# Performance work log

Measured on AMD Instinct MI355X. Metric: run time of the kernel, lower is better.

The kernel has to match this reference:

```python
import jax, jax.numpy as jnp
import numpy as np
from math import sqrt

KEY_DIM = 128
VALUE_DIM = 128
SUMMARY_DIM = 128
QUESTION_NUM = 10000
CONCEPT_NUM = 64
B = 128
S = 128


def setup_inputs() -> dict:
    key = jax.random.key(0)
    ks = jax.random.split(key, 24)
    stdev = 1.0 / sqrt(CONCEPT_NUM + KEY_DIM)

    def lin_w(k, out_f, in_f):
        bound = 1.0 / sqrt(in_f)
        return jax.random.uniform(k, (out_f, in_f), jnp.float32, -bound, bound)

    def lin_b(k, out_f, in_f):
        bound = 1.0 / sqrt(in_f)
        return jax.random.uniform(k, (out_f,), jnp.float32, -bound, bound)

    q_emb = jax.random.normal(ks[0], (QUESTION_NUM + 1, KEY_DIM), jnp.float32)
    q_emb = q_emb.at[0].set(0.0)  # padding_idx = 0
    i_emb = jax.random.normal(ks[1], (2 * QUESTION_NUM + 1, VALUE_DIM), jnp.float32)
    i_emb = i_emb.at[0].set(0.0)

    inp = {
        "right_input": jax.random.randint(ks[2], (B, S), 0, 2 * QUESTION_NUM + 1),
        "wrong_input": jax.random.randint(ks[3], (B, S), 0, 2 * QUESTION_NUM + 1),
        "target_id": jax.random.randint(ks[4], (B,), 0, QUESTION_NUM + 1),
        "q_emb": q_emb,
        "i_emb": i_emb,
        "key_W": lin_w(ks[5], CONCEPT_NUM, KEY_DIM),  # no bias
        "erase_W": lin_w(ks[6], VALUE_DIM, VALUE_DIM),
        "erase_b": lin_b(ks[7], VALUE_DIM, VALUE_DIM),
        "add_W": lin_w(ks[8], VALUE_DIM, VALUE_DIM),
        "add_b": lin_b(ks[9], VALUE_DIM, VALUE_DIM),
        "rsum_W": lin_w(ks[10], SUMMARY_DIM, VALUE_DIM + KEY_DIM),
        "rsum_b": lin_b(ks[11], SUMMARY_DIM, VALUE_DIM + KEY_DIM),
        "wsum_W": lin_w(ks[12], SUMMARY_DIM, VALUE_DIM + KEY_DIM),
        "wsum_b": lin_b(ks[13], SUMMARY_DIM, VALUE_DIM + KEY_DIM),
        "succ_W": lin_w(ks[14], 1, SUMMARY_DIM),
        "succ_b": lin_b(ks[15], 1, SUMMARY_DIM),
        "fail_W": lin_w(ks[16], 1, SUMMARY_DIM),
        "fail_b": lin_b(ks[17], 1, SUMMARY_DIM),
        "diff_W": lin_w(ks[18], 1, KEY_DIM),
        "diff_b": lin_b(ks[19], 1, KEY_DIM),
        "right_mem_init": jax.random.uniform(ks[20], (VALUE_DIM, CONCEPT_NUM), jnp.float32, -stdev, stdev),
        "wrong_mem_init": jax.random.uniform(ks[21], (VALUE_DIM, CONCEPT_NUM), jnp.float32, -stdev, stdev),
    }
    return inp


def reference(right_input, wrong_input, target_id, q_emb, i_emb, key_W,
              erase_W, erase_b, add_W, add_b, rsum_W, rsum_b, wsum_W, wsum_b,
              succ_W, succ_b, fail_W, fail_b, diff_W, diff_b,
              right_mem_init, wrong_mem_init):
    Q = (i_emb.shape[0] - 1) // 2
    batch = right_input.shape[0]

    def corr(qid):  # (B,) -> (B, C) correlation weights
        return jax.nn.softmax(q_emb[qid] @ key_W.T, axis=-1)

    def update(mem, inter):
        # mem: (B, V, C); inter: (B,) interaction ids
        vec = i_emb[inter]                                  # (B, V)
        e = jax.nn.sigmoid(vec @ erase_W.T + erase_b)       # (B, V)
        a = jnp.tanh(vec @ add_W.T + add_b)                 # (B, V)
        qid = inter - Q * (inter > Q).astype(inter.dtype)
        w = corr(qid)                                       # (B, C)
        # erase/add are outer products w (x) e, w (x) a -> (B, V, C)
        return mem * (1.0 - e[:, :, None] * w[:, None, :]) + a[:, :, None] * w[:, None, :]

    def step(carry, xs):
        rm, wm = carry
        ri, wi = xs
        return (update(rm, ri), update(wm, wi)), None

    rm0 = jnp.broadcast_to(right_mem_init, (batch,) + right_mem_init.shape)
    wm0 = jnp.broadcast_to(wrong_mem_init, (batch,) + wrong_mem_init.shape)
    (rm, wm), _ = jax.lax.scan(step, (rm0, wm0), (right_input.T, wrong_input.T))

    qv = q_emb[target_id]                                   # (B, K)
    w_t = corr(target_id)                                   # (B, C)
    right_read = jnp.einsum('bvc,bc->bv', rm, w_t)          # (B, V)
    wrong_read = jnp.einsum('bvc,bc->bv', wm, w_t)

    r_sum = jnp.tanh(jnp.concatenate([right_read, qv], axis=-1) @ rsum_W.T + rsum_b)
    w_sum = jnp.tanh(jnp.concatenate([wrong_read, qv], axis=-1) @ wsum_W.T + wsum_b)

    success_level = jnp.tanh(r_sum @ succ_W.T + succ_b)     # (B, 1)
    failure_level = jnp.tanh(w_sum @ fail_W.T + fail_b)     # (B, 1)
    difficulty_level = jnp.tanh(qv @ diff_W.T + diff_b)     # (B, 1)

    success_count = jnp.sum(jnp.clip(right_input, 0, 1)).astype(jnp.float32)
    failure_count = jnp.sum(jnp.clip(wrong_input, 0, 1)).astype(jnp.float32)

    out = (success_level * jax.nn.sigmoid(success_count)
           + failure_level * jax.nn.sigmoid(failure_count)
           - difficulty_level * 2.0)
    return out
```

## Files before the change

kernel.cpp:

```cpp
#include <hip/hip_runtime.h>
#include <hip/hip_bf16.h>

#define BB 128
#define SS 128
#define VD 128
#define CN 64
#define KD 128
#define QN 10000

typedef __attribute__((ext_vector_type(8))) short bf16x8;
typedef __attribute__((ext_vector_type(4))) float f32x4;

__device__ __forceinline__ float bflo(unsigned int u) { return __uint_as_float(u << 16); }
__device__ __forceinline__ float bfhi(unsigned int u) { return __uint_as_float(u & 0xffff0000u); }
__device__ __forceinline__ unsigned short f2bf(float f) {
    unsigned int x = __float_as_uint(f);
    return (unsigned short)((x + 0x7fffu + ((x >> 16) & 1u)) >> 16);
}
__device__ __forceinline__ unsigned int pk2(float lo, float hi) {
    return (unsigned int)f2bf(lo) | ((unsigned int)f2bf(hi) << 16);
}
__device__ __forceinline__ float fast_tanh(float x) {
    float e = __expf(2.0f * x);
    return 1.0f - 2.0f / (e + 1.0f);
}
__device__ __forceinline__ float fast_sig(float x) {
    return 1.0f / (1.0f + __expf(-x));
}

__global__ __launch_bounds__(256) void k_wcnt(
    const float* __restrict__ erase_W, const float* __restrict__ add_W,
    const float* __restrict__ key_W, unsigned short* __restrict__ Bfrag,
    const int* __restrict__ ri, const int* __restrict__ wi, float* __restrict__ sig)
{
    if (blockIdx.x < 20) {
        const int bid = blockIdx.x * 4 + (threadIdx.x >> 6);
        const int l = threadIdx.x & 63;
        const int n = (bid >> 2) * 16 + (l & 15);
        const int k0 = (bid & 3) * 32 + (l >> 4) * 8;
        const float* src;
        if (n < 128)      src = erase_W + (size_t)n * KD + k0;
        else if (n < 256) src = add_W + (size_t)(n - 128) * KD + k0;
        else              src = key_W + (size_t)(n - 256) * KD + k0;
        float4 fa = ((const float4*)src)[0];
        float4 fb = ((const float4*)src)[1];
        uint4 o = make_uint4(pk2(fa.x, fa.y), pk2(fa.z, fa.w), pk2(fb.x, fb.y), pk2(fb.z, fb.w));
        *(uint4*)(Bfrag + ((size_t)bid * 64 + l) * 8) = o;
    } else {
        __shared__ int sr_s[4], sw_s[4];
        const int t = threadIdx.x;
        const int4* r4 = (const int4*)ri;
        const int4* w4 = (const int4*)wi;
        int sr = 0, sw = 0;
        #pragma unroll 4
        for (int p = 0; p < 16; ++p) {
            int4 a = r4[p * 256 + t];
            int4 b = w4[p * 256 + t];
            sr += (a.x >= 1) + (a.y >= 1) + (a.z >= 1) + (a.w >= 1);
            sw += (b.x >= 1) + (b.y >= 1) + (b.z >= 1) + (b.w >= 1);
        }
        for (int off = 1; off < 64; off <<= 1) { sr += __shfl_xor(sr, off); sw += __shfl_xor(sw, off); }
        int wid = t >> 6;
        if ((t & 63) == 0) { sr_s[wid] = sr; sw_s[wid] = sw; }
        __syncthreads();
        if (t == 0) {
            int SR = sr_s[0]+sr_s[1]+sr_s[2]+sr_s[3];
            int SW = sw_s[0]+sw_s[1]+sw_s[2]+sw_s[3];
            sig[0] = 1.0f / (1.0f + __expf(-(float)SR));
            sig[1] = 1.0f / (1.0f + __expf(-(float)SW));
        }
    }
}

__global__ __launch_bounds__(512, 2) void k_chain(
    const int* __restrict__ ri, const int* __restrict__ wi, const int* __restrict__ tgt,
    const float* __restrict__ q_emb, const float* __restrict__ i_emb,
    const float* __restrict__ key_W,
    const float* __restrict__ erase_b, const float* __restrict__ add_b,
    const unsigned short* __restrict__ Bfrag,
    const float* __restrict__ rmem0, const float* __restrict__ wmem0,
    float* __restrict__ readbuf)
{
    __shared__ __align__(16) unsigned int lds_ea[SS * VD];
    __shared__ __align__(16) char xab[32 * 1024];
    __shared__ __align__(16) float logits[SS * 68];
    __shared__ __align__(16) unsigned short lds_w[SS * CN];
    __shared__ float q_t[KD];
    __shared__ float logit_t[CN];
    __shared__ float wt_lds[CN];
    __shared__ int qid_s[SS], ir_s[SS];
    __shared__ float psum[8 * 64];

    const int t = threadIdx.x;
    const int lane = t & 63;
    const int w = t >> 6;
    const int chain = blockIdx.x;
    const int m = chain >> 7;
    const int b = chain & 127;

    if (t < SS) {
        int inter = (m == 0 ? ri : wi)[b * SS + t];
        ir_s[t] = inter;
        qid_s[t] = (inter > QN) ? inter - QN : inter;
        q_t[t] = q_emb[(size_t)tgt[b] * KD + t];
    }
    __syncthreads();

    {
        const int r0 = t >> 3, o = t & 7;
        #pragma unroll
        for (int h = 0; h < 2; ++h) {
            const int r = r0 + h * 64;
            const float* src = q_emb + (size_t)qid_s[r] * KD + o * 16;
            float4 f0 = ((const float4*)src)[0];
            float4 f1 = ((const float4*)src)[1];
            float4 f2 = ((const float4*)src)[2];
            float4 f3 = ((const float4*)src)[3];
            const int bb = r * 256 + o * 32;
            const int sw = (r & 7) << 4;
            *(uint4*)(xab + (bb ^ sw))        = make_uint4(pk2(f0.x,f0.y), pk2(f0.z,f0.w), pk2(f1.x,f1.y), pk2(f1.z,f1.w));
            *(uint4*)(xab + ((bb + 16) ^ sw)) = make_uint4(pk2(f2.x,f2.y), pk2(f2.z,f2.w), pk2(f3.x,f3.y), pk2(f3.z,f3.w));
        }
        const int c = t >> 3, oct = t & 7;
        const float* kw = key_W + (size_t)c * KD + oct * 16;
        float s = 0.f;
        #pragma unroll
        for (int i = 0; i < 16; ++i) s = fmaf(kw[i], q_t[oct * 16 + i], s);
        s += __shfl_xor(s, 1); s += __shfl_xor(s, 2); s += __shfl_xor(s, 4);
        if (oct == 0) logit_t[c] = s;
    }
    __syncthreads();

    const int rowl = lane & 15;
    const int kb16 = (lane >> 4) * 16;
    const int rb4 = (lane >> 4) * 4;

    {
        if (w == 0) {
            float x = logit_t[lane];
            float mx = x;
            #pragma unroll
            for (int off = 1; off < 64; off <<= 1) mx = fmaxf(mx, __shfl_xor(mx, off));
            float e = __expf(x - mx);
            float ssum = e;
            #pragma unroll
            for (int off = 1; off < 64; off <<= 1) ssum += __shfl_xor(ssum, off);
            wt_lds[lane] = e / ssum;
        }
        bf16x8 afQ[4];
        const int row = w * 16 + rowl;
        #pragma unroll
        for (int kt = 0; kt < 4; ++kt)
            afQ[kt] = *(const bf16x8*)(xab + ((row * 256 + kt * 64 + kb16) ^ ((row & 7) << 4)));
        #pragma unroll
        for (int nt = 0; nt < 4; ++nt) {
            f32x4 acc = {0.f,0.f,0.f,0.f};
            #pragma unroll
            for (int kt = 0; kt < 4; ++kt) {
                bf16x8 bf = *(const bf16x8*)(Bfrag + ((size_t)((16 + nt) * 4 + kt) * 64 + lane) * 8);
                acc = __builtin_amdgcn_mfma_f32_16x16x32_bf16(afQ[kt], bf, acc, 0, 0, 0);
            }
            #pragma unroll
            for (int rr = 0; rr < 4; ++rr)
                logits[(w * 16 + rb4 + rr) * 68 + nt * 16 + rowl] = acc[rr];
        }
    }
    __syncthreads();

    {
        const int r0 = t >> 3, o = t & 7;
        uint4 xi[2][2];
        #pragma unroll
        for (int h = 0; h < 2; ++h) {
            const int r = r0 + h * 64;
            const float* src = i_emb + (size_t)ir_s[r] * KD + o * 16;
            float4 f0 = ((const float4*)src)[0];
            float4 f1 = ((const float4*)src)[1];
            float4 f2 = ((const float4*)src)[2];
            float4 f3 = ((const float4*)src)[3];
            xi[h][0] = make_uint4(pk2(f0.x,f0.y), pk2(f0.z,f0.w), pk2(f1.x,f1.y), pk2(f1.z,f1.w));
            xi[h][1] = make_uint4(pk2(f2.x,f2.y), pk2(f2.z,f2.w), pk2(f3.x,f3.y), pk2(f3.z,f3.w));
        }

        const int rr = t >> 2, q4 = t & 3;
        const float* L = logits + rr * 68 + q4 * 16;
        float4 va = ((const float4*)L)[0];
        float4 vb = ((const float4*)L)[1];
        float4 vc = ((const float4*)L)[2];
        float4 vd = ((const float4*)L)[3];
        float mx = fmaxf(fmaxf(fmaxf(va.x, va.y), fmaxf(va.z, va.w)),
                         fmaxf(fmaxf(vb.x, vb.y), fmaxf(vb.z, vb.w)));
        mx = fmaxf(mx, fmaxf(fmaxf(fmaxf(vc.x, vc.y), fmaxf(vc.z, vc.w)),
                             fmaxf(fmaxf(vd.x, vd.y), fmaxf(vd.z, vd.w))));
        mx = fmaxf(mx, __shfl_xor(mx, 1));
        mx = fmaxf(mx, __shfl_xor(mx, 2));
        float ex[16];
        ex[0] = __expf(va.x - mx); ex[1] = __expf(va.y - mx); ex[2] = __expf(va.z - mx); ex[3] = __expf(va.w - mx);
        ex[4] = __expf(vb.x - mx); ex[5] = __expf(vb.y - mx); ex[6] = __expf(vb.z - mx); ex[7] = __expf(vb.w - mx);
        ex[8] = __expf(vc.x - mx); ex[9] = __expf(vc.y - mx); ex[10] = __expf(vc.z - mx); ex[11] = __expf(vc.w - mx);
        ex[12] = __expf(vd.x - mx); ex[13] = __expf(vd.y - mx); ex[14] = __expf(vd.z - mx); ex[15] = __expf(vd.w - mx);
        float s = 0.f;
        #pragma unroll
        for (int i = 0; i < 16; ++i) s += ex[i];
        s += __shfl_xor(s, 1);
        s += __shfl_xor(s, 2);
        float inv = 1.0f / s;
        uint4 o0 = make_uint4(pk2(ex[0]*inv, ex[1]*inv), pk2(ex[2]*inv, ex[3]*inv),
                              pk2(ex[4]*inv, ex[5]*inv), pk2(ex[6]*inv, ex[7]*inv));
        uint4 o1 = make_uint4(pk2(ex[8]*inv, ex[9]*inv), pk2(ex[10]*inv, ex[11]*inv),
                              pk2(ex[12]*inv, ex[13]*inv), pk2(ex[14]*inv, ex[15]*inv));
        *(uint4*)(lds_w + rr * CN + q4 * 16)     = o0;
        *(uint4*)(lds_w + rr * CN + q4 * 16 + 8) = o1;

        #pragma unroll
        for (int h = 0; h < 2; ++h) {
            const int r = r0 + h * 64;
            const int bb = r * 256 + o * 32;
            const int sw = (r & 7) << 4;
            *(uint4*)(xab + (bb ^ sw))        = xi[h][0];
            *(uint4*)(xab + ((bb + 16) ^ sw)) = xi[h][1];
        }
    }
    __syncthreads();

    {
        bf16x8 afI[4];
        const int row = w * 16 + rowl;
        #pragma unroll
        for (int kt = 0; kt < 4; ++kt)
            afI[kt] = *(const bf16x8*)(xab + ((row * 256 + kt * 64 + kb16) ^ ((row & 7) << 4)));
        #pragma unroll
        for (int ci = 0; ci < 8; ++ci) {
            f32x4 ae = {0.f,0.f,0.f,0.f}, aa = {0.f,0.f,0.f,0.f};
            #pragma unroll
            for (int kt = 0; kt < 4; ++kt) {
                bf16x8 be = *(const bf16x8*)(Bfrag + ((size_t)(ci * 4 + kt) * 64 + lane) * 8);
                bf16x8 ba = *(const bf16x8*)(Bfrag + ((size_t)((8 + ci) * 4 + kt) * 64 + lane) * 8);
                ae = __builtin_amdgcn_mfma_f32_16x16x32_bf16(afI[kt], be, ae, 0, 0, 0);
                aa = __builtin_amdgcn_mfma_f32_16x16x32_bf16(afI[kt], ba, aa, 0, 0, 0);
            }
            const int cc = ci * 16 + rowl;
            const float bvE = erase_b[cc];
            const float bvA = add_b[cc];
            #pragma unroll
            for (int rr = 0; rr < 4; ++rr) {
                float e = fast_sig(ae[rr] + bvE);
                float a = fast_tanh(aa[rr] + bvA);
                lds_ea[(w * 16 + rb4 + rr) * VD + cc] = pk2(e, a);
            }
        }
    }

    const int vhalf = w & 1;
    const int cq = w >> 1;
    const int vg = lane >> 2;
    const int cg = lane & 3;
    const int v0 = vhalf * 64 + vg * 4;
    const int c0 = cq * 16 + cg * 4;
    const float* minit = (m == 0) ? rmem0 : wmem0;
    float mm[4][4];
    #pragma unroll
    for (int j = 0; j < 4; ++j) {
        float4 mi = *(const float4*)(minit + (v0 + j) * CN + c0);
        mm[j][0] = mi.x; mm[j][1] = mi.y; mm[j][2] = mi.z; mm[j][3] = mi.w;
    }
    __syncthreads();

    for (int so = 0; so < 16; ++so) {
        #pragma unroll
        for (int kk = 0; kk < 8; ++kk) {
            const int s = so * 8 + kk;
            uint4 ea = *(const uint4*)(lds_ea + s * VD + v0);
            uint2 wu = *(const uint2*)(lds_w + s * CN + c0);
            float e[4] = { bflo(ea.x), bflo(ea.y), bflo(ea.z), bflo(ea.w) };
            float a[4] = { bfhi(ea.x), bfhi(ea.y), bfhi(ea.z), bfhi(ea.w) };
            float wv[4] = { bflo(wu.x), bfhi(wu.x), bflo(wu.y), bfhi(wu.y) };
            #pragma unroll
            for (int j = 0; j < 4; ++j) {
                #pragma unroll
                for (int k = 0; k < 4; ++k) {
                    float g = fmaf(-e[j], mm[j][k], a[j]);
                    mm[j][k] = fmaf(wv[k], g, mm[j][k]);
                }
            }
        }
    }

    float4 wt = *(const float4*)(wt_lds + c0);
    float p[4];
    #pragma unroll
    for (int j = 0; j < 4; ++j) {
        float x = mm[j][0] * wt.x;
        x = fmaf(mm[j][1], wt.y, x);
        x = fmaf(mm[j][2], wt.z, x);
        x = fmaf(mm[j][3], wt.w, x);
        p[j] = x;
    }
    #pragma unroll
    for (int j = 0; j < 4; ++j) {
        p[j] += __shfl_xor(p[j], 1);
        p[j] += __shfl_xor(p[j], 2);
    }
    if (cg == 0) {
        #pragma unroll
        for (int j = 0; j < 4; ++j) psum[w * 64 + vg * 4 + j] = p[j];
    }
    __syncthreads();
    if (t < 128) {
        const int vh = t >> 6, vl = t & 63;
        float s = psum[(0 * 2 + vh) * 64 + vl] + psum[(1 * 2 + vh) * 64 + vl]
                + psum[(2 * 2 + vh) * 64 + vl] + psum[(3 * 2 + vh) * 64 + vl];
        readbuf[(size_t)chain * VD + t] = s;
    }
}

__global__ __launch_bounds__(256) void k_head(
    const float* __restrict__ readbuf, const int* __restrict__ tgt,
    const float* __restrict__ q_emb,
    const float* __restrict__ rsum_W, const float* __restrict__ rsum_b,
    const float* __restrict__ wsum_W, const float* __restrict__ wsum_b,
    const float* __restrict__ succ_W, const float* __restrict__ succ_b,
    const float* __restrict__ fail_W, const float* __restrict__ fail_b,
    const float* __restrict__ diff_W, const float* __restrict__ diff_b,
    const float* __restrict__ sig, float* __restrict__ out)
{
    __shared__ float xr[256], xw[256];
    __shared__ float part[2][128];
    __shared__ float red_s[6];
    const int t = threadIdx.x;
    const int j = t & 127;
    const int h = t >> 7;
    const int b = blockIdx.x;
    if (h == 0) {
        int tid_ = tgt[b];
        float qv = q_emb[(size_t)tid_ * KD + j];
        xr[j]       = readbuf[(size_t)b * VD + j];
        xr[128 + j] = qv;
        xw[j]       = readbuf[(size_t)(BB + b) * VD + j];
        xw[128 + j] = qv;
    }
    __syncthreads();

    float rs = (h == 0) ? rsum_b[j] : 0.0f;
    float wv = (h == 0) ? wsum_b[j] : 0.0f;
    const float* rw = rsum_W + (size_t)j * 256 + h * 128;
    const float* ww = wsum_W + (size_t)j * 256 + h * 128;
    const float* xrp = xr + h * 128;
    const float* xwp = xw + h * 128;
    #pragma unroll 4
    for (int k = 0; k < 128; ++k) {
        rs = fmaf(rw[k], xrp[k], rs);
        wv = fmaf(ww[k], xwp[k], wv);
    }
    if (h == 1) { part[0][j] = rs; part[1][j] = wv; }
    __syncthreads();
    if (h == 0) {
        rs += part[0][j];
        wv += part[1][j];
        float r_sum = fast_tanh(rs), w_sum = fast_tanh(wv);
        float qv = xr[128 + j];
        float ps = r_sum * succ_W[j];
        float pf = w_sum * fail_W[j];
        float pd = qv    * diff_W[j];
        for (int off = 1; off < 64; off <<= 1) {
            ps += __shfl_xor(ps, off);
            pf += __shfl_xor(pf, off);
            pd += __shfl_xor(pd, off);
        }
        int wid = j >> 6;
        if ((j & 63) == 0) { red_s[wid*3+0] = ps; red_s[wid*3+1] = pf; red_s[wid*3+2] = pd; }
    }
    __syncthreads();
    if (t == 0) {
        float Ps = red_s[0] + red_s[3];
        float Pf = red_s[1] + red_s[4];
        float Pd = red_s[2] + red_s[5];
        float succ = fast_tanh(Ps + succ_b[0]);
        float fail = fast_tanh(Pf + fail_b[0]);
        float diff = fast_tanh(Pd + diff_b[0]);
        out[b] = succ * sig[0] + fail * sig[1] - 2.0f * diff;
    }
}

extern "C" void kernel_launch(void* const* d_in, const int* in_sizes, int n_in,
                              void* d_out, int out_size, void* d_ws, size_t ws_size,
                              hipStream_t stream) {
    const int*   ri      = (const int*)d_in[0];
    const int*   wi      = (const int*)d_in[1];
    const int*   tgt     = (const int*)d_in[2];
    const float* q_emb   = (const float*)d_in[3];
    const float* i_emb   = (const float*)d_in[4];
    const float* key_W   = (const float*)d_in[5];
    const float* erase_W = (const float*)d_in[6];
    const float* erase_b = (const float*)d_in[7];
    const float* add_W   = (const float*)d_in[8];
    const float* add_b   = (const float*)d_in[9];
    const float* rsum_W  = (const float*)d_in[10];
    const float* rsum_b  = (const float*)d_in[11];
    const float* wsum_W  = (const float*)d_in[12];
    const float* wsum_b  = (const float*)d_in[13];
    const float* succ_W  = (const float*)d_in[14];
    const float* succ_b  = (const float*)d_in[15];
    const float* fail_W  = (const float*)d_in[16];
    const float* fail_b  = (const float*)d_in[17];
    const float* diff_W  = (const float*)d_in[18];
    const float* diff_b  = (const float*)d_in[19];
    const float* rmem0   = (const float*)d_in[20];
    const float* wmem0   = (const float*)d_in[21];

    char* ws = (char*)d_ws;
    float*          readbuf = (float*)(ws + 0);
    unsigned short* Bfrag   = (unsigned short*)(ws + 131072);
    float*          sig     = (float*)(ws + 212992);
    float*          out     = (float*)d_out;

    hipLaunchKernelGGL(k_wcnt, dim3(21), dim3(256), 0, stream,
        erase_W, add_W, key_W, Bfrag, ri, wi, sig);
    hipLaunchKernelGGL(k_chain, dim3(256), dim3(512), 0, stream,
        ri, wi, tgt, q_emb, i_emb, key_W, erase_b, add_b, Bfrag,
        rmem0, wmem0, readbuf);
    hipLaunchKernelGGL(k_head, dim3(128), dim3(256), 0, stream,
        readbuf, tgt, q_emb, rsum_W, rsum_b, wsum_W, wsum_b,
        succ_W, succ_b, fail_W, fail_b, diff_W, diff_b, sig, out);
}
```

Measured before the change: 50.58 us.

## Double k_chain block to 1024 threads and alias LDS buffers

Raises the chain kernel's block from 512 to 1024 threads, so each thread in the serial memory-update loop holds 2x4 state elements instead of 4x4, halving the per-thread dependency chain. The MFMA stages are split so waves share row tiles but divide the column tiles, and the xab/logits/lds_ea buffers are overlaid in one shared region to fit the larger block. The psum reduction is replaced by a 16-lane shuffle reduction with direct global writes. Costs include an extra barrier, more register pressure under the tighter launch bound, and more LDS loads per useful FMA in the recurrence.

Result: slower. 52.14 us (+3.1%).

```diff
diff --git a/kernel.cpp b/kernel.cpp
--- a/kernel.cpp
+++ b/kernel.cpp
@@ -72,7 +72,7 @@
     }
 }
 
-__global__ __launch_bounds__(512, 2) void k_chain(
+__global__ __launch_bounds__(1024, 4) void k_chain(
     const int* __restrict__ ri, const int* __restrict__ wi, const int* __restrict__ tgt,
     const float* __restrict__ q_emb, const float* __restrict__ i_emb,
     const float* __restrict__ key_W,
@@ -81,15 +81,16 @@
     const float* __restrict__ rmem0, const float* __restrict__ wmem0,
     float* __restrict__ readbuf)
 {
-    __shared__ __align__(16) unsigned int lds_ea[SS * VD];
-    __shared__ __align__(16) char xab[32 * 1024];
-    __shared__ __align__(16) float logits[SS * 68];
+    __shared__ __align__(16) char U[32768 + 34816];
     __shared__ __align__(16) unsigned short lds_w[SS * CN];
     __shared__ float q_t[KD];
     __shared__ float logit_t[CN];
     __shared__ float wt_lds[CN];
     __shared__ int qid_s[SS], ir_s[SS];
-    __shared__ float psum[8 * 64];
+
+    char* xab = U;
+    float* logits = (float*)(U + 32768);
+    unsigned int* lds_ea = (unsigned int*)U;
 
     const int t = threadIdx.x;
     const int lane = t & 63;
@@ -107,33 +108,32 @@
     __syncthreads();
 
     {
-        const int r0 = t >> 3, o = t & 7;
-        #pragma unroll
-        for (int h = 0; h < 2; ++h) {
-            const int r = r0 + h * 64;
-            const float* src = q_emb + (size_t)qid_s[r] * KD + o * 16;
-            float4 f0 = ((const float4*)src)[0];
-            float4 f1 = ((const float4*)src)[1];
-            float4 f2 = ((const float4*)src)[2];
-            float4 f3 = ((const float4*)src)[3];
-            const int bb = r * 256 + o * 32;
-            const int sw = (r & 7) << 4;
-            *(uint4*)(xab + (bb ^ sw))        = make_uint4(pk2(f0.x,f0.y), pk2(f0.z,f0.w), pk2(f1.x,f1.y), pk2(f1.z,f1.w));
-            *(uint4*)(xab + ((bb + 16) ^ sw)) = make_uint4(pk2(f2.x,f2.y), pk2(f2.z,f2.w), pk2(f3.x,f3.y), pk2(f3.z,f3.w));
-        }
-        const int c = t >> 3, oct = t & 7;
-        const float* kw = key_W + (size_t)c * KD + oct * 16;
-        float s = 0.f;
-        #pragma unroll
-        for (int i = 0; i < 16; ++i) s = fmaf(kw[i], q_t[oct * 16 + i], s);
-        s += __shfl_xor(s, 1); s += __shfl_xor(s, 2); s += __shfl_xor(s, 4);
-        if (oct == 0) logit_t[c] = s;
+        const int r = t >> 3, o = t & 7;
+        const float* src = q_emb + (size_t)qid_s[r] * KD + o * 16;
+        float4 f0 = ((const float4*)src)[0];
+        float4 f1 = ((const float4*)src)[1];
+        float4 f2 = ((const float4*)src)[2];
+        float4 f3 = ((const float4*)src)[3];
+        const int bb = r * 256 + o * 32;
+        const int sw = (r & 7) << 4;
+        *(uint4*)(xab + (bb ^ sw))        = make_uint4(pk2(f0.x,f0.y), pk2(f0.z,f0.w), pk2(f1.x,f1.y), pk2(f1.z,f1.w));
+        *(uint4*)(xab + ((bb + 16) ^ sw)) = make_uint4(pk2(f2.x,f2.y), pk2(f2.z,f2.w), pk2(f3.x,f3.y), pk2(f3.z,f3.w));
+        if (t < 512) {
+            const int c = t >> 3, oct = t & 7;
+            const float* kw = key_W + (size_t)c * KD + oct * 16;
+            float s = 0.f;
+            #pragma unroll
+            for (int i = 0; i < 16; ++i) s = fmaf(kw[i], q_t[oct * 16 + i], s);
+            s += __shfl_xor(s, 1); s += __shfl_xor(s, 2); s += __shfl_xor(s, 4);
+            if (oct == 0) logit_t[c] = s;
+        }
     }
     __syncthreads();
 
     const int rowl = lane & 15;
     const int kb16 = (lane >> 4) * 16;
     const int rb4 = (lane >> 4) * 4;
+    const int rt = w & 7;
 
     {
         if (w == 0) {
@@ -148,12 +148,14 @@
             wt_lds[lane] = e / ssum;
         }
         bf16x8 afQ[4];
-        const int row = w * 16 + rowl;
+        const int row = rt * 16 + rowl;
         #pragma unroll
         for (int kt = 0; kt < 4; ++kt)
             afQ[kt] = *(const bf16x8*)(xab + ((row * 256 + kt * 64 + kb16) ^ ((row & 7) << 4)));
-        #pragma unroll
-        for (int nt = 0; nt < 4; ++nt) {
+        const int nt0 = (w >> 3) * 2;
+        #pragma unroll
+        for (int ni = 0; ni < 2; ++ni) {
+            const int nt = nt0 + ni;
             f32x4 acc = {0.f,0.f,0.f,0.f};
             #pragma unroll
             for (int kt = 0; kt < 4; ++kt) {
@@ -162,75 +164,56 @@
             }
             #pragma unroll
             for (int rr = 0; rr < 4; ++rr)
-                logits[(w * 16 + rb4 + rr) * 68 + nt * 16 + rowl] = acc[rr];
-        }
-    }
-    __syncthreads();
-
-    {
-        const int r0 = t >> 3, o = t & 7;
-        uint4 xi[2][2];
-        #pragma unroll
-        for (int h = 0; h < 2; ++h) {
-            const int r = r0 + h * 64;
-            const float* src = i_emb + (size_t)ir_s[r] * KD + o * 16;
-            float4 f0 = ((const float4*)src)[0];
-            float4 f1 = ((const float4*)src)[1];
-            float4 f2 = ((const float4*)src)[2];
-            float4 f3 = ((const float4*)src)[3];
-            xi[h][0] = make_uint4(pk2(f0.x,f0.y), pk2(f0.z,f0.w), pk2(f1.x,f1.y), pk2(f1.z,f1.w));
-            xi[h][1] = make_uint4(pk2(f2.x,f2.y), pk2(f2.z,f2.w), pk2(f3.x,f3.y), pk2(f3.z,f3.w));
-        }
-
-        const int rr = t >> 2, q4 = t & 3;
-        const float* L = logits + rr * 68 + q4 * 16;
+                logits[(rt * 16 + rb4 + rr) * 68 + nt * 16 + rowl] = acc[rr];
+        }
+    }
+    __syncthreads();
+
+    {
+        const int rr = t >> 3, q = t & 7;
+        const float* L = logits + rr * 68 + q * 8;
         float4 va = ((const float4*)L)[0];
         float4 vb = ((const float4*)L)[1];
-        float4 vc = ((const float4*)L)[2];
-        float4 vd = ((const float4*)L)[3];
         float mx = fmaxf(fmaxf(fmaxf(va.x, va.y), fmaxf(va.z, va.w)),
                          fmaxf(fmaxf(vb.x, vb.y), fmaxf(vb.z, vb.w)));
-        mx = fmaxf(mx, fmaxf(fmaxf(fmaxf(vc.x, vc.y), fmaxf(vc.z, vc.w)),
-                             fmaxf(fmaxf(vd.x, vd.y), fmaxf(vd.z, vd.w))));
         mx = fmaxf(mx, __shfl_xor(mx, 1));
         mx = fmaxf(mx, __shfl_xor(mx, 2));
-        float ex[16];
-        ex[0] = __expf(va.x - mx); ex[1] = __expf(va.y - mx); ex[2] = __expf(va.z - mx); ex[3] = __expf(va.w - mx);
-        ex[4] = __expf(vb.x - mx); ex[5] = __expf(vb.y - mx); ex[6] = __expf(vb.z - mx); ex[7] = __expf(vb.w - mx);
-        ex[8] = __expf(vc.x - mx); ex[9] = __expf(vc.y - mx); ex[10] = __expf(vc.z - mx); ex[11] = __expf(vc.w - mx);
-        ex[12] = __expf(vd.x - mx); ex[13] = __expf(vd.y - mx); ex[14] = __expf(vd.z - mx); ex[15] = __expf(vd.w - mx);
-        float s = 0.f;
-        #pragma unroll
-        for (int i = 0; i < 16; ++i) s += ex[i];
-        s += __shfl_xor(s, 1);
-        s += __shfl_xor(s, 2);
+        mx = fmaxf(mx, __shfl_xor(mx, 4));
+        float e0 = __expf(va.x - mx), e1 = __expf(va.y - mx), e2 = __expf(va.z - mx), e3 = __expf(va.w - mx);
+        float e4 = __expf(vb.x - mx), e5 = __expf(vb.y - mx), e6 = __expf(vb.z - mx), e7 = __expf(vb.w - mx);
+        float s = e0 + e1 + e2 + e3 + e4 + e5 + e6 + e7;
+        s += __shfl_xor(s, 1); s += __shfl_xor(s, 2); s += __shfl_xor(s, 4);
         float inv = 1.0f / s;
-        uint4 o0 = make_uint4(pk2(ex[0]*inv, ex[1]*inv), pk2(ex[2]*inv, ex[3]*inv),
-                              pk2(ex[4]*inv, ex[5]*inv), pk2(ex[6]*inv, ex[7]*inv));
-        uint4 o1 = make_uint4(pk2(ex[8]*inv, ex[9]*inv), pk2(ex[10]*inv, ex[11]*inv),
-                              pk2(ex[12]*inv, ex[13]*inv), pk2(ex[14]*inv, ex[15]*inv));
-        *(uint4*)(lds_w + rr * CN + q4 * 16)     = o0;
-        *(uint4*)(lds_w + rr * CN + q4 * 16 + 8) = o1;
-
-        #pragma unroll
-        for (int h = 0; h < 2; ++h) {
-            const int r = r0 + h * 64;
-            const int bb = r * 256 + o * 32;
-            const int sw = (r & 7) << 4;
-            *(uint4*)(xab + (bb ^ sw))        = xi[h][0];
-            *(uint4*)(xab + ((bb + 16) ^ sw)) = xi[h][1];
-        }
-    }
-    __syncthreads();
-
-    {
-        bf16x8 afI[4];
-        const int row = w * 16 + rowl;
+        uint4 o = make_uint4(pk2(e0*inv, e1*inv), pk2(e2*inv, e3*inv),
+                             pk2(e4*inv, e5*inv), pk2(e6*inv, e7*inv));
+        *(uint4*)(lds_w + rr * CN + q * 8) = o;
+
+        const float* src = i_emb + (size_t)ir_s[rr] * KD + q * 16;
+        float4 f0 = ((const float4*)src)[0];
+        float4 f1 = ((const float4*)src)[1];
+        float4 f2 = ((const float4*)src)[2];
+        float4 f3 = ((const float4*)src)[3];
+        const int bb = rr * 256 + q * 32;
+        const int sw = (rr & 7) << 4;
+        *(uint4*)(xab + (bb ^ sw))        = make_uint4(pk2(f0.x,f0.y), pk2(f0.z,f0.w), pk2(f1.x,f1.y), pk2(f1.z,f1.w));
+        *(uint4*)(xab + ((bb + 16) ^ sw)) = make_uint4(pk2(f2.x,f2.y), pk2(f2.z,f2.w), pk2(f3.x,f3.y), pk2(f3.z,f3.w));
+    }
+    __syncthreads();
+
+    bf16x8 afI[4];
+    {
+        const int row = rt * 16 + rowl;
         #pragma unroll
         for (int kt = 0; kt < 4; ++kt)
             afI[kt] = *(const bf16x8*)(xab + ((row * 256 + kt * 64 + kb16) ^ ((row & 7) << 4)));
-        #pragma unroll
-        for (int ci = 0; ci < 8; ++ci) {
+    }
+    __syncthreads();
+
+    {
+        const int ci0 = (w >> 3) * 4;
+        #pragma unroll
+        for (int ii = 0; ii < 4; ++ii) {
+            const int ci = ci0 + ii;
             f32x4 ae = {0.f,0.f,0.f,0.f}, aa = {0.f,0.f,0.f,0.f};
             #pragma unroll
             for (int kt = 0; kt < 4; ++kt) {
@@ -246,71 +229,61 @@
             for (int rr = 0; rr < 4; ++rr) {
                 float e = fast_sig(ae[rr] + bvE);
                 float a = fast_tanh(aa[rr] + bvA);
-                lds_ea[(w * 16 + rb4 + rr) * VD + cc] = pk2(e, a);
+                lds_ea[(rt * 16 + rb4 + rr) * VD + cc] = pk2(e, a);
             }
         }
     }
 
-    const int vhalf = w & 1;
-    const int cq = w >> 1;
-    const int vg = lane >> 2;
-    const int cg = lane & 3;
-    const int v0 = vhalf * 64 + vg * 4;
-    const int c0 = cq * 16 + cg * 4;
+    const int v0 = (t >> 4) * 2;
+    const int c0 = (t & 15) * 4;
     const float* minit = (m == 0) ? rmem0 : wmem0;
-    float mm[4][4];
-    #pragma unroll
-    for (int j = 0; j < 4; ++j) {
-        float4 mi = *(const float4*)(minit + (v0 + j) * CN + c0);
-        mm[j][0] = mi.x; mm[j][1] = mi.y; mm[j][2] = mi.z; mm[j][3] = mi.w;
-    }
-    __syncthreads();
-
+    float mm0[4], mm1[4];
+    {
+        float4 a0 = *(const float4*)(minit + (v0 + 0) * CN + c0);
+        float4 a1 = *(const float4*)(minit + (v0 + 1) * CN + c0);
+        mm0[0] = a0.x; mm0[1] = a0.y; mm0[2] = a0.z; mm0[3] = a0.w;
+        mm1[0] = a1.x; mm1[1] = a1.y; mm1[2] = a1.z; mm1[3] = a1.w;
+    }
+    __syncthreads();
+
+    const unsigned int* ea_base = lds_ea + v0;
+    const unsigned short* w_base = lds_w + c0;
     for (int so = 0; so < 16; ++so) {
         #pragma unroll
         for (int kk = 0; kk < 8; ++kk) {
             const int s = so * 8 + kk;
-            uint4 ea = *(const uint4*)(lds_ea + s * VD + v0);
-            uint2 wu = *(const uint2*)(lds_w + s * CN + c0);
-            float e[4] = { bflo(ea.x), bflo(ea.y), bflo(ea.z), bflo(ea.w) };
-            float a[4] = { bfhi(ea.x), bfhi(ea.y), bfhi(ea.z), bfhi(ea.w) };
-            float wv[4] = { bflo(wu.x), bfhi(wu.x), bflo(wu.y), bfhi(wu.y) };
-            #pragma unroll
-            for (int j = 0; j < 4; ++j) {
-                #pragma unroll
-                for (int k = 0; k < 4; ++k) {
-                    float g = fmaf(-e[j], mm[j][k], a[j]);
-                    mm[j][k] = fmaf(wv[k], g, mm[j][k]);
-                }
-            }
-        }
-    }
-
-    float4 wt = *(const float4*)(wt_lds + c0);
-    float p[4];
-    #pragma unroll
-    for (int j = 0; j < 4; ++j) {
-        float x = mm[j][0] * wt.x;
-        x = fmaf(mm[j][1], wt.y, x);
-        x = fmaf(mm[j][2], wt.z, x);
-        x = fmaf(mm[j][3], wt.w, x);
-        p[j] = x;
-    }
-    #pragma unroll
-    for (int j = 0; j < 4; ++j) {
-        p[j] += __shfl_xor(p[j], 1);
-        p[j] += __shfl_xor(p[j], 2);
-    }
-    if (cg == 0) {
-        #pragma unroll
-        for (int j = 0; j < 4; ++j) psum[w * 64 + vg * 4 + j] = p[j];
-    }
-    __syncthreads();
-    if (t < 128) {
-        const int vh = t >> 6, vl = t & 63;
-        float s = psum[(0 * 2 + vh) * 64 + vl] + psum[(1 * 2 + vh) * 64 + vl]
-                + psum[(2 * 2 + vh) * 64 + vl] + psum[(3 * 2 + vh) * 64 + vl];
-        readbuf[(size_t)chain * VD + t] = s;
+            uint2 ea = *(const uint2*)(ea_base + s * VD);
+            uint2 wu = *(const uint2*)(w_base + s * CN);
+            float e0 = bflo(ea.x), a0 = bfhi(ea.x);
+            float e1 = bflo(ea.y), a1 = bfhi(ea.y);
+            float w0 = bflo(wu.x), w1 = bfhi(wu.x), w2 = bflo(wu.y), w3 = bfhi(wu.y);
+            float g;
+            g = fmaf(-e0, mm0[0], a0); mm0[0] = fmaf(w0, g, mm0[0]);
+            g = fmaf(-e0, mm0[1], a0); mm0[1] = fmaf(w1, g, mm0[1]);
+            g = fmaf(-e0, mm0[2], a0); mm0[2] = fmaf(w2, g, mm0[2]);
+            g = fmaf(-e0, mm0[3], a0); mm0[3] = fmaf(w3, g, mm0[3]);
+            g = fmaf(-e1, mm1[0], a1); mm1[0] = fmaf(w0, g, mm1[0]);
+            g = fmaf(-e1, mm1[1], a1); mm1[1] = fmaf(w1, g, mm1[1]);
+            g = fmaf(-e1, mm1[2], a1); mm1[2] = fmaf(w2, g, mm1[2]);
+            g = fmaf(-e1, mm1[3], a1); mm1[3] = fmaf(w3, g, mm1[3]);
+        }
+    }
+
+    {
+        float4 wt = *(const float4*)(wt_lds + c0);
+        float p0 = mm0[0] * wt.x;
+        p0 = fmaf(mm0[1], wt.y, p0); p0 = fmaf(mm0[2], wt.z, p0); p0 = fmaf(mm0[3], wt.w, p0);
+        float p1 = mm1[0] * wt.x;
+        p1 = fmaf(mm1[1], wt.y, p1); p1 = fmaf(mm1[2], wt.z, p1); p1 = fmaf(mm1[3], wt.w, p1);
+        #pragma unroll
+        for (int off = 1; off < 16; off <<= 1) {
+            p0 += __shfl_xor(p0, off);
+            p1 += __shfl_xor(p1, off);
+        }
+        if ((t & 15) == 0) {
+            readbuf[(size_t)chain * VD + v0]     = p0;
+            readbuf[(size_t)chain * VD + v0 + 1] = p1;
+        }
     }
 }
 
@@ -416,7 +389,7 @@
 
     hipLaunchKernelGGL(k_wcnt, dim3(21), dim3(256), 0, stream,
         erase_W, add_W, key_W, Bfrag, ri, wi, sig);
-    hipLaunchKernelGGL(k_chain, dim3(256), dim3(512), 0, stream,
+    hipLaunchKernelGGL(k_chain, dim3(256), dim3(1024), 0, stream,
         ri, wi, tgt, q_emb, i_emb, key_W, erase_b, add_b, Bfrag,
         rmem0, wmem0, readbuf);
     hipLaunchKernelGGL(k_head, dim3(128), dim3(256), 0, stream,
```

## Double k_chain block to 1024 threads, splitting gather and MFMA phases

Applied to the files above, without the earlier changes.

Launches k_chain with 1024 threads instead of 512. The embedding gathers, softmax and MFMA projection phases are split across 16 waves, each doing half the previous per-thread work, while the serial memory recurrence still runs on the first 512 threads. The aim is to cut latency in the gather- and MFMA-bound prologue that runs before the recurrence. It also replaces the hand-written bf16 rounding with the library packed float2-to-bf16 conversion. Raising launch bounds to (1024,4) may tighten the register budget and cause spills in the recurrence, and half the threads sit idle during the main loop.

Result: no change. 50.16 us (median of 2 runs) (-0.8%).

```diff
diff --git a/kernel.cpp b/kernel.cpp
--- a/kernel.cpp
+++ b/kernel.cpp
@@ -13,12 +13,9 @@
 
 __device__ __forceinline__ float bflo(unsigned int u) { return __uint_as_float(u << 16); }
 __device__ __forceinline__ float bfhi(unsigned int u) { return __uint_as_float(u & 0xffff0000u); }
-__device__ __forceinline__ unsigned short f2bf(float f) {
-    unsigned int x = __float_as_uint(f);
-    return (unsigned short)((x + 0x7fffu + ((x >> 16) & 1u)) >> 16);
-}
-__device__ __forceinline__ unsigned int pk2(float lo, float hi) {
-    return (unsigned int)f2bf(lo) | ((unsigned int)f2bf(hi) << 16);
+__device__ __forceinline__ unsigned int cvtpk(float lo, float hi) {
+    __hip_bfloat162 h2 = __float22bfloat162_rn(make_float2(lo, hi));
+    unsigned int r; __builtin_memcpy(&r, &h2, 4); return r;
 }
 __device__ __forceinline__ float fast_tanh(float x) {
     float e = __expf(2.0f * x);
@@ -33,9 +30,10 @@
     const float* __restrict__ key_W, unsigned short* __restrict__ Bfrag,
     const int* __restrict__ ri, const int* __restrict__ wi, float* __restrict__ sig)
 {
+    const int t = threadIdx.x;
     if (blockIdx.x < 20) {
-        const int bid = blockIdx.x * 4 + (threadIdx.x >> 6);
-        const int l = threadIdx.x & 63;
+        const int bid = blockIdx.x * 4 + (t >> 6);
+        const int l = t & 63;
         const int n = (bid >> 2) * 16 + (l & 15);
         const int k0 = (bid & 3) * 32 + (l >> 4) * 8;
         const float* src;
@@ -44,11 +42,10 @@
         else              src = key_W + (size_t)(n - 256) * KD + k0;
         float4 fa = ((const float4*)src)[0];
         float4 fb = ((const float4*)src)[1];
-        uint4 o = make_uint4(pk2(fa.x, fa.y), pk2(fa.z, fa.w), pk2(fb.x, fb.y), pk2(fb.z, fb.w));
+        uint4 o = make_uint4(cvtpk(fa.x, fa.y), cvtpk(fa.z, fa.w), cvtpk(fb.x, fb.y), cvtpk(fb.z, fb.w));
         *(uint4*)(Bfrag + ((size_t)bid * 64 + l) * 8) = o;
     } else {
         __shared__ int sr_s[4], sw_s[4];
-        const int t = threadIdx.x;
         const int4* r4 = (const int4*)ri;
         const int4* w4 = (const int4*)wi;
         int sr = 0, sw = 0;
@@ -72,7 +69,7 @@
     }
 }
 
-__global__ __launch_bounds__(512, 2) void k_chain(
+__global__ __launch_bounds__(1024, 4) void k_chain(
     const int* __restrict__ ri, const int* __restrict__ wi, const int* __restrict__ tgt,
     const float* __restrict__ q_emb, const float* __restrict__ i_emb,
     const float* __restrict__ key_W,
@@ -107,33 +104,32 @@
     __syncthreads();
 
     {
-        const int r0 = t >> 3, o = t & 7;
-        #pragma unroll
-        for (int h = 0; h < 2; ++h) {
-            const int r = r0 + h * 64;
-            const float* src = q_emb + (size_t)qid_s[r] * KD + o * 16;
-            float4 f0 = ((const float4*)src)[0];
-            float4 f1 = ((const float4*)src)[1];
-            float4 f2 = ((const float4*)src)[2];
-            float4 f3 = ((const float4*)src)[3];
-            const int bb = r * 256 + o * 32;
-            const int sw = (r & 7) << 4;
-            *(uint4*)(xab + (bb ^ sw))        = make_uint4(pk2(f0.x,f0.y), pk2(f0.z,f0.w), pk2(f1.x,f1.y), pk2(f1.z,f1.w));
-            *(uint4*)(xab + ((bb + 16) ^ sw)) = make_uint4(pk2(f2.x,f2.y), pk2(f2.z,f2.w), pk2(f3.x,f3.y), pk2(f3.z,f3.w));
-        }
-        const int c = t >> 3, oct = t & 7;
-        const float* kw = key_W + (size_t)c * KD + oct * 16;
-        float s = 0.f;
-        #pragma unroll
-        for (int i = 0; i < 16; ++i) s = fmaf(kw[i], q_t[oct * 16 + i], s);
-        s += __shfl_xor(s, 1); s += __shfl_xor(s, 2); s += __shfl_xor(s, 4);
-        if (oct == 0) logit_t[c] = s;
+        const int r = t >> 3, o = t & 7;
+        const float* src = q_emb + (size_t)qid_s[r] * KD + o * 16;
+        float4 f0 = ((const float4*)src)[0];
+        float4 f1 = ((const float4*)src)[1];
+        float4 f2 = ((const float4*)src)[2];
+        float4 f3 = ((const float4*)src)[3];
+        const int bb = r * 256 + o * 32;
+        const int sw = (r & 7) << 4;
+        *(uint4*)(xab + (bb ^ sw))        = make_uint4(cvtpk(f0.x,f0.y), cvtpk(f0.z,f0.w), cvtpk(f1.x,f1.y), cvtpk(f1.z,f1.w));
+        *(uint4*)(xab + ((bb + 16) ^ sw)) = make_uint4(cvtpk(f2.x,f2.y), cvtpk(f2.z,f2.w), cvtpk(f3.x,f3.y), cvtpk(f3.z,f3.w));
+        if (t < 512) {
+            const int c = t >> 3, oct = t & 7;
+            const float* kw = key_W + (size_t)c * KD + oct * 16;
+            float s = 0.f;
+            #pragma unroll
+            for (int i = 0; i < 16; ++i) s = fmaf(kw[i], q_t[oct * 16 + i], s);
+            s += __shfl_xor(s, 1); s += __shfl_xor(s, 2); s += __shfl_xor(s, 4);
+            if (oct == 0) logit_t[c] = s;
+        }
     }
     __syncthreads();
 
     const int rowl = lane & 15;
     const int kb16 = (lane >> 4) * 16;
     const int rb4 = (lane >> 4) * 4;
+    const int rt = w & 7;
 
     {
         if (w == 0) {
@@ -148,12 +144,14 @@
             wt_lds[lane] = e / ssum;
         }
         bf16x8 afQ[4];
-        const int row = w * 16 + rowl;
+        const int row = rt * 16 + rowl;
         #pragma unroll
         for (int kt = 0; kt < 4; ++kt)
             afQ[kt] = *(const bf16x8*)(xab + ((row * 256 + kt * 64 + kb16) ^ ((row & 7) << 4)));
-        #pragma unroll
-        for (int nt = 0; nt < 4; ++nt) {
+        const int nt0 = (w >> 3) * 2;
+        #pragma unroll
+        for (int ni = 0; ni < 2; ++ni) {
+            const int nt = nt0 + ni;
             f32x4 acc = {0.f,0.f,0.f,0.f};
             #pragma unroll
             for (int kt = 0; kt < 4; ++kt) {
@@ -162,75 +160,52 @@
             }
             #pragma unroll
             for (int rr = 0; rr < 4; ++rr)
-                logits[(w * 16 + rb4 + rr) * 68 + nt * 16 + rowl] = acc[rr];
+                logits[(rt * 16 + rb4 + rr) * 68 + nt * 16 + rowl] = acc[rr];
         }
     }
     __syncthreads();
 
     {
-        const int r0 = t >> 3, o = t & 7;
-        uint4 xi[2][2];
-        #pragma unroll
-        for (int h = 0; h < 2; ++h) {
-            const int r = r0 + h * 64;
-            const float* src = i_emb + (size_t)ir_s[r] * KD + o * 16;
-            float4 f0 = ((const float4*)src)[0];
-            float4 f1 = ((const float4*)src)[1];
-            float4 f2 = ((const float4*)src)[2];
-            float4 f3 = ((const float4*)src)[3];
-            xi[h][0] = make_uint4(pk2(f0.x,f0.y), pk2(f0.z,f0.w), pk2(f1.x,f1.y), pk2(f1.z,f1.w));
-            xi[h][1] = make_uint4(pk2(f2.x,f2.y), pk2(f2.z,f2.w), pk2(f3.x,f3.y), pk2(f3.z,f3.w));
-        }
-
-        const int rr = t >> 2, q4 = t & 3;
-        const float* L = logits + rr * 68 + q4 * 16;
+        const int rr = t >> 3, q = t & 7;
+        const float* L = logits + rr * 68 + q * 8;
         float4 va = ((const float4*)L)[0];
         float4 vb = ((const float4*)L)[1];
-        float4 vc = ((const float4*)L)[2];
-        float4 vd = ((const float4*)L)[3];
         float mx = fmaxf(fmaxf(fmaxf(va.x, va.y), fmaxf(va.z, va.w)),
                          fmaxf(fmaxf(vb.x, vb.y), fmaxf(vb.z, vb.w)));
-        mx = fmaxf(mx, fmaxf(fmaxf(fmaxf(vc.x, vc.y), fmaxf(vc.z, vc.w)),
-                             fmaxf(fmaxf(vd.x, vd.y), fmaxf(vd.z, vd.w))));
         mx = fmaxf(mx, __shfl_xor(mx, 1));
         mx = fmaxf(mx, __shfl_xor(mx, 2));
-        float ex[16];
-        ex[0] = __expf(va.x - mx); ex[1] = __expf(va.y - mx); ex[2] = __expf(va.z - mx); ex[3] = __expf(va.w - mx);
-        ex[4] = __expf(vb.x - mx); ex[5] = __expf(vb.y - mx); ex[6] = __expf(vb.z - mx); ex[7] = __expf(vb.w - mx);
-        ex[8] = __expf(vc.x - mx); ex[9] = __expf(vc.y - mx); ex[10] = __expf(vc.z - mx); ex[11] = __expf(vc.w - mx);
-        ex[12] = __expf(vd.x - mx); ex[13] = __expf(vd.y - mx); ex[14] = __expf(vd.z - mx); ex[15] = __expf(vd.w - mx);
-        float s = 0.f;
-        #pragma unroll
-        for (int i = 0; i < 16; ++i) s += ex[i];
-        s += __shfl_xor(s, 1);
-        s += __shfl_xor(s, 2);
+        mx = fmaxf(mx, __shfl_xor(mx, 4));
+        float e0 = __expf(va.x - mx), e1 = __expf(va.y - mx), e2 = __expf(va.z - mx), e3 = __expf(va.w - mx);
+        float e4 = __expf(vb.x - mx), e5 = __expf(vb.y - mx), e6 = __expf(vb.z - mx), e7 = __expf(vb.w - mx);
+        float s = e0 + e1 + e2 + e3 + e4 + e5 + e6 + e7;
+        s += __shfl_xor(s, 1); s += __shfl_xor(s, 2); s += __shfl_xor(s, 4);
         float inv = 1.0f / s;
-        uint4 o0 = make_uint4(pk2(ex[0]*inv, ex[1]*inv), pk2(ex[2]*inv, ex[3]*inv),
-                              pk2(ex[4]*inv, ex[5]*inv), pk2(ex[6]*inv, ex[7]*inv));
-        uint4 o1 = make_uint4(pk2(ex[8]*inv, ex[9]*inv), pk2(ex[10]*inv, ex[11]*inv),
-                              pk2(ex[12]*inv, ex[13]*inv), pk2(ex[14]*inv, ex[15]*inv));
-        *(uint4*)(lds_w + rr * CN + q4 * 16)     = o0;
-        *(uint4*)(lds_w + rr * CN + q4 * 16 + 8) = o1;
-
-        #pragma unroll
-        for (int h = 0; h < 2; ++h) {
-            const int r = r0 + h * 64;
-            const int bb = r * 256 + o * 32;
-            const int sw = (r & 7) << 4;
-            *(uint4*)(xab + (bb ^ sw))        = xi[h][0];
-            *(uint4*)(xab + ((bb + 16) ^ sw)) = xi[h][1];
-        }
+        uint4 o = make_uint4(cvtpk(e0*inv, e1*inv), cvtpk(e2*inv, e3*inv),
+                             cvtpk(e4*inv, e5*inv), cvtpk(e6*inv, e7*inv));
+        *(uint4*)(lds_w + rr * CN + q * 8) = o;
+
+        const float* src = i_emb + (size_t)ir_s[rr] * KD + q * 16;
+        float4 f0 = ((const float4*)src)[0];
+        float4 f1 = ((const float4*)src)[1];
+        float4 f2 = ((const float4*)src)[2];
+        float4 f3 = ((const float4*)src)[3];
+        const int bb = rr * 256 + q * 32;
+        const int sw = (rr & 7) << 4;
+        *(uint4*)(xab + (bb ^ sw))        = make_uint4(cvtpk(f0.x,f0.y), cvtpk(f0.z,f0.w), cvtpk(f1.x,f1.y), cvtpk(f1.z,f1.w));
+        *(uint4*)(xab + ((bb + 16) ^ sw)) = make_uint4(cvtpk(f2.x,f2.y), cvtpk(f2.z,f2.w), cvtpk(f3.x,f3.y), cvtpk(f3.z,f3.w));
     }
     __syncthreads();
 
     {
         bf16x8 afI[4];
-        const int row = w * 16 + rowl;
+        const int row = rt * 16 + rowl;
         #pragma unroll
         for (int kt = 0; kt < 4; ++kt)
             afI[kt] = *(const bf16x8*)(xab + ((row * 256 + kt * 64 + kb16) ^ ((row & 7) << 4)));
-        #pragma unroll
-        for (int ci = 0; ci < 8; ++ci) {
+        const int ci0 = (w >> 3) * 4;
+        #pragma unroll
+        for (int ii = 0; ii < 4; ++ii) {
+            const int ci = ci0 + ii;
             f32x4 ae = {0.f,0.f,0.f,0.f}, aa = {0.f,0.f,0.f,0.f};
             #pragma unroll
             for (int kt = 0; kt < 4; ++kt) {
@@ -246,64 +221,71 @@
             for (int rr = 0; rr < 4; ++rr) {
                 float e = fast_sig(ae[rr] + bvE);
                 float a = fast_tanh(aa[rr] + bvA);
-                lds_ea[(w * 16 + rb4 + rr) * VD + cc] = pk2(e, a);
+                lds_ea[(rt * 16 + rb4 + rr) * VD + cc] = cvtpk(e, a);
             }
         }
     }
 
-    const int vhalf = w & 1;
-    const int cq = w >> 1;
+    const int w2 = w & 7;
+    const int vhalf = w2 & 1;
+    const int cq = w2 >> 1;
     const int vg = lane >> 2;
     const int cg = lane & 3;
     const int v0 = vhalf * 64 + vg * 4;
     const int c0 = cq * 16 + cg * 4;
-    const float* minit = (m == 0) ? rmem0 : wmem0;
+
     float mm[4][4];
-    #pragma unroll
-    for (int j = 0; j < 4; ++j) {
-        float4 mi = *(const float4*)(minit + (v0 + j) * CN + c0);
-        mm[j][0] = mi.x; mm[j][1] = mi.y; mm[j][2] = mi.z; mm[j][3] = mi.w;
-    }
-    __syncthreads();
-
-    for (int so = 0; so < 16; ++so) {
-        #pragma unroll
-        for (int kk = 0; kk < 8; ++kk) {
-            const int s = so * 8 + kk;
-            uint4 ea = *(const uint4*)(lds_ea + s * VD + v0);
-            uint2 wu = *(const uint2*)(lds_w + s * CN + c0);
-            float e[4] = { bflo(ea.x), bflo(ea.y), bflo(ea.z), bflo(ea.w) };
-            float a[4] = { bfhi(ea.x), bfhi(ea.y), bfhi(ea.z), bfhi(ea.w) };
-            float wv[4] = { bflo(wu.x), bfhi(wu.x), bflo(wu.y), bfhi(wu.y) };
-            #pragma unroll
-            for (int j = 0; j < 4; ++j) {
+    if (t < 512) {
+        const float* minit = (m == 0) ? rmem0 : wmem0;
+        #pragma unroll
+        for (int j = 0; j < 4; ++j) {
+            float4 mi = *(const float4*)(minit + (v0 + j) * CN + c0);
+            mm[j][0] = mi.x; mm[j][1] = mi.y; mm[j][2] = mi.z; mm[j][3] = mi.w;
+        }
+    }
+    __syncthreads();
+
+    if (t < 512) {
+        for (int so = 0; so < 16; ++so) {
+            const unsigned int* eap = lds_ea + (so * 8) * VD + v0;
+            const unsigned short* wp = lds_w + (so * 8) * CN + c0;
+            #pragma unroll
+            for (int kk = 0; kk < 8; ++kk) {
+                uint4 ea = *(const uint4*)(eap + kk * VD);
+                uint2 wu = *(const uint2*)(wp + kk * CN);
+                float e[4] = { bflo(ea.x), bflo(ea.y), bflo(ea.z), bflo(ea.w) };
+                float a[4] = { bfhi(ea.x), bfhi(ea.y), bfhi(ea.z), bfhi(ea.w) };
+                float wv[4] = { bflo(wu.x), bfhi(wu.x), bflo(wu.y), bfhi(wu.y) };
                 #pragma unroll
-                for (int k = 0; k < 4; ++k) {
-                    float g = fmaf(-e[j], mm[j][k], a[j]);
-                    mm[j][k] = fmaf(wv[k], g, mm[j][k]);
+                for (int j = 0; j < 4; ++j) {
+                    #pragma unroll
+                    for (int k = 0; k < 4; ++k) {
+                        float g = fmaf(-e[j], mm[j][k], a[j]);
+                        mm[j][k] = fmaf(wv[k], g, mm[j][k]);
+                    }
                 }
             }
         }
-    }
-
-    float4 wt = *(const float4*)(wt_lds + c0);
-    float p[4];
-    #pragma unroll
-    for (int j = 0; j < 4; ++j) {
-        float x = mm[j][0] * wt.x;
-        x = fmaf(mm[j][1], wt.y, x);
-        x = fmaf(mm[j][2], wt.z, x);
-        x = fmaf(mm[j][3], wt.w, x);
-        p[j] = x;
-    }
-    #pragma unroll
-    for (int j = 0; j < 4; ++j) {
-        p[j] += __shfl_xor(p[j], 1);
-        p[j] += __shfl_xor(p[j], 2);
-    }
-    if (cg == 0) {
-        #pragma unroll
-        for (int j = 0; j < 4; ++j) psum[w * 64 + vg * 4 + j] = p[j];
+
+        float4 wt = *(const float4*)(wt_lds + c0);
+        float p[4];
+        #pragma unroll
+        for (int j = 0; j < 4; ++j) {
+            float x = mm[j][0] * wt.x;
+            x = fmaf(mm[j][1], wt.y, x);
+            x = fmaf(mm[j][2], wt.z, x);
+            x = fmaf(mm[j][3], wt.w, x);
+            p[j] = x;
+        }
+        #pragma unroll
+        for (int j = 0; j < 4; ++j) {
+            p[j] += __shfl_xor(p[j], 1);
+            p[j] += __shfl_xor(p[j], 2);
+        }
+        if (cg == 0) {
+            #pragma unroll
+            for (int j = 0; j < 4; ++j) psum[w2 * 64 + vg * 4 + j] = p[j];
+        }
     }
     __syncthreads();
     if (t < 128) {
@@ -416,7 +398,7 @@
 
     hipLaunchKernelGGL(k_wcnt, dim3(21), dim3(256), 0, stream,
         erase_W, add_W, key_W, Bfrag, ri, wi, sig);
-    hipLaunchKernelGGL(k_chain, dim3(256), dim3(512), 0, stream,
+    hipLaunchKernelGGL(k_chain, dim3(256), dim3(1024), 0, stream,
         ri, wi, tgt, q_emb, i_emb, key_W, erase_b, add_b, Bfrag,
         rmem0, wmem0, readbuf);
     hipLaunchKernelGGL(k_head, dim3(128), dim3(256), 0, stream,
```
